# Kernel tuning notes

Hardware: AMD Instinct MI355X
Metric: run time of the kernel (lower is better)

## Reference

```python
import jax, jax.numpy as jnp
import numpy as np

D_MODEL = 2048
N_HEADS = 32
N_KV = 8
D_K = D_MODEL // N_HEADS  # 64
N_REP = N_HEADS // N_KV   # 4


def setup_inputs() -> dict:
    key = jax.random.key(0)
    ks = jax.random.split(key, 5)
    B, T = 2, 2048
    s = 0.02
    return {
        "x": jax.random.normal(ks[0], (B, T, D_MODEL), dtype=jnp.float32),
        "Wq": jax.random.normal(ks[1], (D_MODEL, D_MODEL), dtype=jnp.float32) * s,
        "Wk": jax.random.normal(ks[2], (N_KV * D_K, D_MODEL), dtype=jnp.float32) * s,
        "Wv": jax.random.normal(ks[3], (N_KV * D_K, D_MODEL), dtype=jnp.float32) * s,
        "Wo": jax.random.normal(ks[4], (D_MODEL, D_MODEL), dtype=jnp.float32) * s,
    }


def reference(x, Wq, Wk, Wv, Wo):
    B, T, C = x.shape
    # projections (torch Linear: x @ W.T)
    Q = (x @ Wq.T).reshape(B, T, N_KV, N_REP, D_K)  # group query heads by kv group
    K = (x @ Wk.T).reshape(B, T, N_KV, D_K)
    V = (x @ Wv.T).reshape(B, T, N_KV, D_K)
    scale = 1.0 / jnp.sqrt(jnp.asarray(D_K, dtype=x.dtype))
    # scores: (B, n_kv, n_rep, T, T) == repeated-KV scores without materializing repeats
    scores = jnp.einsum('btgrd,bsgd->bgrts', Q, K) * scale
    causal_mask = jnp.triu(jnp.ones((T, T), dtype=bool), k=1)
    scores = jnp.where(causal_mask, -jnp.inf, scores)
    attn = jax.nn.softmax(scores, axis=-1)
    out = jnp.einsum('bgrts,bsgd->btgrd', attn, V).reshape(B, T, C)
    return out @ Wo.T
```

## Files before the change

### kernel.cpp

```cpp
#include <hip/hip_runtime.h>
#include <hip/hip_bf16.h>

typedef __attribute__((ext_vector_type(8))) short bf16x8;
typedef __attribute__((ext_vector_type(4))) float floatx4;

constexpr int D_MODEL = 2048;
constexpr int N_HEADS = 32;
constexpr int N_KV    = 8;
constexpr int B_      = 2;
constexpr int T_      = 2048;
constexpr int BT      = B_ * T_;
constexpr int NQKV    = 3072;

constexpr float Q_SCALE = 0.18033688011112042f;

__device__ __forceinline__ unsigned short f2bf(float f) {
    __hip_bfloat16 h = __float2bfloat16(f);
    return *reinterpret_cast<unsigned short*>(&h);
}

__device__ __forceinline__ unsigned bfpack_rn(float a, float b) {
    unsigned ba = __builtin_bit_cast(unsigned, a);
    unsigned bb = __builtin_bit_cast(unsigned, b);
    return ((ba + 0x8000u) >> 16) | ((bb + 0x8000u) & 0xFFFF0000u);
}

__device__ __forceinline__ void gll16(const void* g, void* l) {
    typedef const __attribute__((address_space(1))) unsigned int* gp_t;
    typedef __attribute__((address_space(3))) unsigned int* lp_t;
    __builtin_amdgcn_global_load_lds((gp_t)g, (lp_t)l, 16, 0, 0);
}

__global__ __launch_bounds__(256) void cvt_all(
        const float* __restrict__ x,  const float* __restrict__ wq,
        const float* __restrict__ wk, const float* __restrict__ wv,
        unsigned short* __restrict__ dst) {
    size_t i4 = (size_t)blockIdx.x * 256 + threadIdx.x;
    size_t e = i4 * 4;
    const float* src; size_t off;
    if (e < 8388608)        { src = x;  off = 0; }
    else if (e < 12582912)  { src = wq; off = 8388608; }
    else if (e < 13631488)  { src = wk; off = 12582912; }
    else                    { src = wv; off = 13631488; }
    float4 f = *reinterpret_cast<const float4*>(src + (e - off));
    unsigned short u[4] = {f2bf(f.x), f2bf(f.y), f2bf(f.z), f2bf(f.w)};
    reinterpret_cast<uint2*>(dst)[i4] = *reinterpret_cast<const uint2*>(u);
}

__global__ __launch_bounds__(256) void cvt_bf16(
        const float* __restrict__ src, unsigned short* __restrict__ dst, int n4) {
    int i = blockIdx.x * 256 + threadIdx.x;
    if (i < n4) {
        float4 f = reinterpret_cast<const float4*>(src)[i];
        unsigned short u[4] = {f2bf(f.x), f2bf(f.y), f2bf(f.z), f2bf(f.w)};
        reinterpret_cast<uint2*>(dst)[i] = *reinterpret_cast<const uint2*>(u);
    }
}

template<bool C_F32, bool SCALEQ, bool FUSEV>
__global__ __launch_bounds__(256) void gemm128(
        const unsigned short* __restrict__ A,
        const unsigned short* __restrict__ Bb,
        void* __restrict__ Cp,
        unsigned short* __restrict__ Vtp,
        int M, int N, int K) {
    __shared__ unsigned short As[128 * 64];
    __shared__ unsigned short Bs[128 * 64];
    const int t = threadIdx.x;
    const int wave = t >> 6, lane = t & 63;
    const int l16 = lane & 15, quad = lane >> 4;
    const int wm = (wave & 1) * 64, wn = (wave >> 1) * 64;

    const int gx = gridDim.x;
    int bid = blockIdx.y * gx + blockIdx.x;
    const int cpx = (gx * gridDim.y) >> 3;
    bid = (bid & 7) * cpx + (bid >> 3);
    const int mtile = (bid / gx) * 128, ntile = (bid % gx) * 128;

    floatx4 acc[4][4] = {};

    for (int k0 = 0; k0 < K; k0 += 64) {
        __syncthreads();
#pragma unroll
        for (int c = 0; c < 4; c++) {
            int s = (c * 4 + wave) * 64 + lane;
            int row = s >> 3, k8 = (s & 7) ^ (row & 7);
            gll16(&A[(size_t)(mtile + row) * K + k0 + k8 * 8], &As[(c * 4 + wave) * 512]);
            gll16(&Bb[(size_t)(ntile + row) * K + k0 + k8 * 8], &Bs[(c * 4 + wave) * 512]);
        }
        __syncthreads();
#pragma unroll
        for (int kc = 0; kc < 2; kc++) {
            bf16x8 af[4], bfr[4];
#pragma unroll
            for (int i = 0; i < 4; i++) {
                int arow = wm + i * 16 + l16;
                af[i] = *reinterpret_cast<const bf16x8*>(
                    &As[(arow * 8 + ((kc * 4 + quad) ^ (arow & 7))) * 8]);
                int brow = wn + i * 16 + l16;
                bfr[i] = *reinterpret_cast<const bf16x8*>(
                    &Bs[(brow * 8 + ((kc * 4 + quad) ^ (brow & 7))) * 8]);
            }
#pragma unroll
            for (int i = 0; i < 4; i++)
#pragma unroll
                for (int jn = 0; jn < 4; jn++)
                    acc[i][jn] = __builtin_amdgcn_mfma_f32_16x16x32_bf16(
                        af[i], bfr[jn], acc[i][jn], 0, 0, 0);
        }
    }
    float cscale = (SCALEQ && ntile < 2048) ? Q_SCALE : 1.0f;
#pragma unroll
    for (int i = 0; i < 4; i++)
#pragma unroll
        for (int jn = 0; jn < 4; jn++) {
            int col = ntile + wn + jn * 16 + l16;
#pragma unroll
            for (int r = 0; r < 4; r++) {
                int row = mtile + wm + i * 16 + quad * 4 + r;
                if constexpr (C_F32) {
                    ((float*)Cp)[(size_t)row * N + col] = acc[i][jn][r];
                } else {
                    unsigned short v = f2bf(acc[i][jn][r] * cscale);
                    ((unsigned short*)Cp)[(size_t)row * N + col] = v;
                    if constexpr (FUSEV)
                        if (col >= 2560) {
                            int d = col - 2560;
                            int gg = d >> 6, dd = d & 63;
                            int bb = row >> 11, tok = row & 2047;
                            Vtp[(((size_t)bb * 8 + gg) * 64 + dd) * T_ + tok] = v;
                        }
                }
            }
        }
}

__global__ __launch_bounds__(512, 4) void attn7(
        const unsigned short* __restrict__ QKV,
        const unsigned short* __restrict__ Vt,
        unsigned short* __restrict__ O) {
    __shared__ unsigned short Ks[64 * 64];
    __shared__ unsigned short Vs[64 * 64];
    __shared__ unsigned short Ps[8][16 * 72];
    const int j  = blockIdx.x;
    const int bh = blockIdx.y;
    const int b = bh >> 5, h = bh & 31;
    const int g = h >> 2;
    const int t = threadIdx.x, wave = t >> 6, lane = t & 63;
    const int l16 = lane & 15, quad = lane >> 4;

    bf16x8 ones;
#pragma unroll
    for (int i = 0; i < 8; i++) ones[i] = (short)0x3F80;

    const int srow = t >> 3;
    const int sk8  = (t & 7) ^ (srow & 7);
    const unsigned short* kbase =
        QKV + (size_t)(b * T_ + srow) * NQKV + 2048 + g * 64 + sk8 * 8;
    const unsigned short* vbase =
        Vt + ((size_t)(b * 8 + g) * 64 + srow) * T_ + sk8 * 8;
    unsigned short* kdst = &Ks[wave * 512];
    unsigned short* vdst = &Vs[wave * 512];

    for (int pp = 0; pp < 2; pp++) {
        const int qtl = pp ? (15 - j) : j;
        const int q0  = qtl * 128;
        const int qlo = q0 + wave * 16;

        const unsigned short* qptr =
            QKV + (size_t)(b * T_ + qlo + l16) * NQKV + h * 64;
        bf16x8 qf0 = *reinterpret_cast<const bf16x8*>(qptr + quad * 8);
        bf16x8 qf1 = *reinterpret_cast<const bf16x8*>(qptr + 32 + quad * 8);

        floatx4 o[4] = {};
        floatx4 lacc = {};

        const unsigned short* kp = kbase;
        const unsigned short* vp = vbase;

        const int nkt = 2 * qtl + 2;
        for (int kt = 0; kt < nkt; kt++) {
            const int kb = kt * 64;
            __syncthreads();
            gll16(kp, kdst);
            gll16(vp, vdst);
            kp += 64 * NQKV;
            vp += 64;
            __syncthreads();

            if (kb > qlo + 15) continue;
            const bool needmask = (kb + 63 > qlo);

#pragma unroll
            for (int km = 0; km < 4; km++) {
                int krow = km * 16 + l16;
                bf16x8 k0 = *reinterpret_cast<const bf16x8*>(
                    &Ks[(krow * 8 + (quad ^ (krow & 7))) * 8]);
                bf16x8 k1 = *reinterpret_cast<const bf16x8*>(
                    &Ks[(krow * 8 + ((4 + quad) ^ (krow & 7))) * 8]);
                floatx4 z = {};
                __builtin_amdgcn_s_setprio(1);
                z = __builtin_amdgcn_mfma_f32_16x16x32_bf16(k0, qf0, z, 0, 0, 0);
                z = __builtin_amdgcn_mfma_f32_16x16x32_bf16(k1, qf1, z, 0, 0, 0);
                __builtin_amdgcn_s_setprio(0);
                float p[4];
#pragma unroll
                for (int r = 0; r < 4; r++)
                    p[r] = __builtin_amdgcn_exp2f(z[r]);
                if (needmask) {
                    int qq = qlo + l16;
#pragma unroll
                    for (int r = 0; r < 4; r++)
                        if ((kb + km * 16 + quad * 4 + r) > qq) p[r] = 0.f;
                }
                uint2 w;
                w.x = bfpack_rn(p[0], p[1]);
                w.y = bfpack_rn(p[2], p[3]);
                *reinterpret_cast<uint2*>(
                    &Ps[wave][l16 * 72 + km * 16 + quad * 4]) = w;
            }

            bf16x8 pf[2];
            __builtin_amdgcn_s_setprio(1);
#pragma unroll
            for (int ks = 0; ks < 2; ks++)
                pf[ks] = *reinterpret_cast<const bf16x8*>(
                    &Ps[wave][l16 * 72 + ks * 32 + quad * 8]);
            lacc = __builtin_amdgcn_mfma_f32_16x16x32_bf16(pf[0], ones, lacc, 0, 0, 0);
            lacc = __builtin_amdgcn_mfma_f32_16x16x32_bf16(pf[1], ones, lacc, 0, 0, 0);
#pragma unroll
            for (int dt = 0; dt < 4; dt++) {
                int vrow = dt * 16 + l16;
                bf16x8 v0 = *reinterpret_cast<const bf16x8*>(
                    &Vs[(vrow * 8 + (quad ^ (vrow & 7))) * 8]);
                bf16x8 v1 = *reinterpret_cast<const bf16x8*>(
                    &Vs[(vrow * 8 + ((4 + quad) ^ (vrow & 7))) * 8]);
                o[dt] = __builtin_amdgcn_mfma_f32_16x16x32_bf16(pf[0], v0, o[dt], 0, 0, 0);
                o[dt] = __builtin_amdgcn_mfma_f32_16x16x32_bf16(pf[1], v1, o[dt], 0, 0, 0);
            }
            __builtin_amdgcn_s_setprio(0);
        }

#pragma unroll
        for (int r = 0; r < 4; r++) {
            float inv = 1.0f / lacc[r];
            int row = b * T_ + qlo + quad * 4 + r;
#pragma unroll
            for (int dt = 0; dt < 4; dt++)
                O[(size_t)row * D_MODEL + h * 64 + dt * 16 + l16] =
                    f2bf(o[dt][r] * inv);
        }
    }
}

extern "C" void kernel_launch(void* const* d_in, const int* in_sizes, int n_in,
                              void* d_out, int out_size, void* d_ws, size_t ws_size,
                              hipStream_t stream) {
    const float* x  = (const float*)d_in[0];
    const float* Wq = (const float*)d_in[1];
    const float* Wk = (const float*)d_in[2];
    const float* Wv = (const float*)d_in[3];
    const float* Wo = (const float*)d_in[4];

    unsigned short* xb   = (unsigned short*)d_ws;
    unsigned short* Wqkv = xb + (size_t)BT * D_MODEL;
    unsigned short* QKVo = Wqkv + (size_t)NQKV * D_MODEL;
    unsigned short* Vt   = QKVo + (size_t)BT * NQKV;
    unsigned short* Aw   = xb;
    unsigned short* Wob  = Wqkv;

    dim3 blk(256);
    cvt_all<<<dim3(14336), blk, 0, stream>>>(x, Wq, Wk, Wv, xb);
    gemm128<false, true, true><<<dim3(NQKV / 128, BT / 128), blk, 0, stream>>>(
        xb, Wqkv, QKVo, Vt, BT, NQKV, D_MODEL);
    cvt_bf16<<<dim3(D_MODEL * D_MODEL / 4 / 256), blk, 0, stream>>>(
        Wo, Wob, D_MODEL * D_MODEL / 4);
    attn7<<<dim3(8, B_ * N_HEADS), dim3(512), 0, stream>>>(QKVo, Vt, Aw);
    gemm128<true, false, false><<<dim3(D_MODEL / 128, BT / 128), blk, 0, stream>>>(
        Aw, Wob, d_out, nullptr, BT, D_MODEL, D_MODEL);
}
```

Before: 287.8 us.

## Add 256x256 double-buffered LDS-staged GEMM for the QKV projection

Adds a new gemm256 kernel with 256x256 output tiles and 512 threads, used for the fused QKV projection. It double-buffers the A and B tiles in LDS via direct global-to-LDS loads with an XOR swizzle, and uses explicit vmcnt waits so loads for step n+2 overlap MFMA work on step n. It also splits each K-step's MFMAs into two halves around a barrier and raises wave priority during the MFMA phases. The aim is more data reuse per tile and hiding memory latency. In exchange, 128KB of LDS per block and only 192 blocks may leave some CUs idle, and register pressure rises.

```diff
diff --git a/kernel.cpp b/kernel.cpp
--- a/kernel.cpp
+++ b/kernel.cpp
@@ -57,12 +57,133 @@
     }
 }
 
-template<bool C_F32, bool SCALEQ, bool FUSEV>
+template<bool SCALEQ, bool FUSEV>
+__global__ __launch_bounds__(512, 2) void gemm256(
+        const unsigned short* __restrict__ A,
+        const unsigned short* __restrict__ Bb,
+        unsigned short* __restrict__ Cp,
+        unsigned short* __restrict__ Vtp,
+        int M, int N, int K) {
+    __shared__ unsigned short As[2][256 * 64];
+    __shared__ unsigned short Bs[2][256 * 64];
+    const int t = threadIdx.x;
+    const int wave = t >> 6, lane = t & 63;
+    const int l16 = lane & 15, quad = lane >> 4;
+    const int wm = (wave & 1) * 128, wn = (wave >> 1) * 64;
+
+    const int gx = gridDim.x;
+    int bid = blockIdx.y * gx + blockIdx.x;
+    const int cpx = (gx * gridDim.y) >> 3;
+    bid = (bid & 7) * cpx + (bid >> 3);
+    const int mtile = (bid / gx) * 256, ntile = (bid % gx) * 256;
+
+    auto stage = [&](int kt, int bi) {
+        const int k0 = kt * 64;
+#pragma unroll
+        for (int c = 0; c < 4; c++) {
+            int s = c * 512 + t;
+            int row = s >> 3, k8 = (s & 7) ^ (row & 7);
+            gll16(&A[(size_t)(mtile + row) * K + k0 + k8 * 8],
+                  &As[bi][(c * 8 + wave) * 512]);
+            gll16(&Bb[(size_t)(ntile + row) * K + k0 + k8 * 8],
+                  &Bs[bi][(c * 8 + wave) * 512]);
+        }
+    };
+
+    floatx4 acc[8][4] = {};
+
+    const int NKT = K >> 6;
+    stage(0, 0);
+    stage(1, 1);
+
+    for (int n = 0; n < NKT; ++n) {
+        const int cur = n & 1;
+        if (n == NKT - 1) asm volatile("s_waitcnt vmcnt(0)" ::: "memory");
+        else              asm volatile("s_waitcnt vmcnt(8)" ::: "memory");
+        __builtin_amdgcn_s_barrier();
+        asm volatile("" ::: "memory");
+
+        bf16x8 bfr[4][2], aflo[4][2], afhi[4][2];
+#pragma unroll
+        for (int nf = 0; nf < 4; nf++)
+#pragma unroll
+            for (int kc = 0; kc < 2; kc++) {
+                int brow = wn + nf * 16 + l16;
+                bfr[nf][kc] = *reinterpret_cast<const bf16x8*>(
+                    &Bs[cur][(brow * 8 + ((kc * 4 + quad) ^ (brow & 7))) * 8]);
+            }
+#pragma unroll
+        for (int mf = 0; mf < 4; mf++)
+#pragma unroll
+            for (int kc = 0; kc < 2; kc++) {
+                int arow = wm + mf * 16 + l16;
+                aflo[mf][kc] = *reinterpret_cast<const bf16x8*>(
+                    &As[cur][(arow * 8 + ((kc * 4 + quad) ^ (arow & 7))) * 8]);
+            }
+        __builtin_amdgcn_s_setprio(1);
+#pragma unroll
+        for (int mf = 0; mf < 4; mf++)
+#pragma unroll
+            for (int nf = 0; nf < 4; nf++)
+#pragma unroll
+                for (int kc = 0; kc < 2; kc++)
+                    acc[mf][nf] = __builtin_amdgcn_mfma_f32_16x16x32_bf16(
+                        aflo[mf][kc], bfr[nf][kc], acc[mf][nf], 0, 0, 0);
+        __builtin_amdgcn_s_setprio(0);
+#pragma unroll
+        for (int mf = 0; mf < 4; mf++)
+#pragma unroll
+            for (int kc = 0; kc < 2; kc++) {
+                int arow = wm + (mf + 4) * 16 + l16;
+                afhi[mf][kc] = *reinterpret_cast<const bf16x8*>(
+                    &As[cur][(arow * 8 + ((kc * 4 + quad) ^ (arow & 7))) * 8]);
+            }
+        asm volatile("s_waitcnt lgkmcnt(0)" ::: "memory");
+        __builtin_amdgcn_sched_barrier(0);
+        __builtin_amdgcn_s_barrier();
+        asm volatile("" ::: "memory");
+
+        if (n + 2 < NKT) stage(n + 2, cur);
+
+        __builtin_amdgcn_s_setprio(1);
+#pragma unroll
+        for (int mf = 0; mf < 4; mf++)
+#pragma unroll
+            for (int nf = 0; nf < 4; nf++)
+#pragma unroll
+                for (int kc = 0; kc < 2; kc++)
+                    acc[mf + 4][nf] = __builtin_amdgcn_mfma_f32_16x16x32_bf16(
+                        afhi[mf][kc], bfr[nf][kc], acc[mf + 4][nf], 0, 0, 0);
+        __builtin_amdgcn_s_setprio(0);
+    }
+
+    float cscale = (SCALEQ && ntile < 2048) ? Q_SCALE : 1.0f;
+#pragma unroll
+    for (int i = 0; i < 8; i++)
+#pragma unroll
+        for (int jn = 0; jn < 4; jn++) {
+            int col = ntile + wn + jn * 16 + l16;
+#pragma unroll
+            for (int r = 0; r < 4; r++) {
+                int row = mtile + wm + i * 16 + quad * 4 + r;
+                unsigned short v = f2bf(acc[i][jn][r] * cscale);
+                Cp[(size_t)row * N + col] = v;
+                if constexpr (FUSEV)
+                    if (col >= 2560) {
+                        int d = col - 2560;
+                        int gg = d >> 6, dd = d & 63;
+                        int bb = row >> 11, tok = row & 2047;
+                        Vtp[(((size_t)bb * 8 + gg) * 64 + dd) * T_ + tok] = v;
+                    }
+            }
+        }
+}
+
+template<bool C_F32, bool SCALEQ>
 __global__ __launch_bounds__(256) void gemm128(
         const unsigned short* __restrict__ A,
         const unsigned short* __restrict__ Bb,
         void* __restrict__ Cp,
-        unsigned short* __restrict__ Vtp,
         int M, int N, int K) {
     __shared__ unsigned short As[128 * 64];
     __shared__ unsigned short Bs[128 * 64];
@@ -118,19 +239,11 @@
 #pragma unroll
             for (int r = 0; r < 4; r++) {
                 int row = mtile + wm + i * 16 + quad * 4 + r;
-                if constexpr (C_F32) {
+                if constexpr (C_F32)
                     ((float*)Cp)[(size_t)row * N + col] = acc[i][jn][r];
-                } else {
-                    unsigned short v = f2bf(acc[i][jn][r] * cscale);
-                    ((unsigned short*)Cp)[(size_t)row * N + col] = v;
-                    if constexpr (FUSEV)
-                        if (col >= 2560) {
-                            int d = col - 2560;
-                            int gg = d >> 6, dd = d & 63;
-                            int bb = row >> 11, tok = row & 2047;
-                            Vtp[(((size_t)bb * 8 + gg) * 64 + dd) * T_ + tok] = v;
-                        }
-                }
+                else
+                    ((unsigned short*)Cp)[(size_t)row * N + col] =
+                        f2bf(acc[i][jn][r] * cscale);
             }
         }
 }
@@ -271,11 +384,11 @@
 
     dim3 blk(256);
     cvt_all<<<dim3(14336), blk, 0, stream>>>(x, Wq, Wk, Wv, xb);
-    gemm128<false, true, true><<<dim3(NQKV / 128, BT / 128), blk, 0, stream>>>(
+    gemm256<true, true><<<dim3(NQKV / 256, BT / 256), dim3(512), 0, stream>>>(
         xb, Wqkv, QKVo, Vt, BT, NQKV, D_MODEL);
     cvt_bf16<<<dim3(D_MODEL * D_MODEL / 4 / 256), blk, 0, stream>>>(
         Wo, Wob, D_MODEL * D_MODEL / 4);
     attn7<<<dim3(8, B_ * N_HEADS), dim3(512), 0, stream>>>(QKVo, Vt, Aw);
-    gemm128<true, false, false><<<dim3(D_MODEL / 128, BT / 128), blk, 0, stream>>>(
-        Aw, Wob, d_out, nullptr, BT, D_MODEL, D_MODEL);
-}
+    gemm128<true, false><<<dim3(D_MODEL / 128, BT / 128), blk, 0, stream>>>(
+        Aw, Wob, d_out, BT, D_MODEL, D_MODEL);
+}
```

After: 295.6 us. 2.7% more time.
